# Optimization experiments

Hardware: AMD Instinct MI355X
Metric: run time of the kernel (lower is better)

## Reference

```python
import jax, jax.numpy as jnp
import numpy as np

BATCH, D_IN, D_OUT = 2048, 1024, 4096


def setup_inputs() -> dict:
    key = jax.random.key(0)
    kx, kw = jax.random.split(key)
    x = jax.random.normal(kx, (BATCH, D_IN), dtype=jnp.float32)
    W = jax.random.normal(kw, (D_IN, D_OUT), dtype=jnp.float32)  # nn.Parameter init: N(0,1)
    return {"x": x, "W": W}


def reference(x, W):
    # out[b,o] = -1/2 * sum_i (x[b,i] - W[i,o])^2
    # instead of materializing the [B, O, I] broadcast tensor.
    x_sq = jnp.sum(x * x, axis=1, keepdims=True)          # [B, 1]
    w_sq = jnp.sum(W * W, axis=0, keepdims=True)          # [1, O]
    xw = jnp.matmul(x, W)                                  # [B, O] GEMM
    return -0.5 * (x_sq - 2.0 * xw + w_sq)
```

## Files before the change

kernel.cpp:

```cpp
#include <hip/hip_runtime.h>
#include <stdint.h>

#define BATCH 2048
#define DIN   1024
#define DOUT  4096


__device__ __forceinline__ ushort f2bf(float f) {
    uint32_t u = __float_as_uint(f);
    u += 0x7fffu + ((u >> 16) & 1u);
    return (ushort)(u >> 16);
}

__device__ __forceinline__ void async_copy16(const void* gsrc, void* ldst) {
    __builtin_amdgcn_global_load_lds(
        reinterpret_cast<uint32_t __attribute__((address_space(1)))*>(
            reinterpret_cast<uintptr_t>(gsrc)),
        reinterpret_cast<uint32_t __attribute__((address_space(3)))*>(
            reinterpret_cast<uintptr_t>(ldst)),
        16, 0, 0);
}

typedef __bf16 bf16x8 __attribute__((ext_vector_type(8)));
typedef float  f32x4  __attribute__((ext_vector_type(4)));

__global__ __launch_bounds__(256) void prep_fused(const float* __restrict__ x,
                                                  const float* __restrict__ W,
                                                  ushort* __restrict__ xb,
                                                  float* __restrict__ xsq,
                                                  ushort* __restrict__ wbt,
                                                  float* __restrict__ wsqp) {
    __shared__ float tile[64][65];
    const int b = blockIdx.x;
    if (b < 256) {
        const int o0 = (b >> 2) * 64;
        const int jb = b & 3;
        const int tx = threadIdx.x & 63;
        const int ty = threadIdx.x >> 6;
        float ssq = 0.f;
        for (int sub = 0; sub < 4; ++sub) {
            const int i0 = jb * 256 + sub * 64;
            if (sub) __syncthreads();
            #pragma unroll
            for (int r = ty; r < 64; r += 4) {
                const float v = W[(size_t)(i0 + r) * DOUT + o0 + tx];
                tile[r][tx] = v;
                ssq += v * v;
            }
            __syncthreads();
            #pragma unroll
            for (int r = ty; r < 64; r += 4)
                wbt[(size_t)(o0 + r) * DIN + i0 + tx] = f2bf(tile[tx][r]);
        }
        __syncthreads();
        tile[ty][tx] = ssq;
        __syncthreads();
        if (ty == 0)
            wsqp[(size_t)jb * DOUT + o0 + tx] =
                tile[0][tx] + tile[1][tx] + tile[2][tx] + tile[3][tx];
    } else {
        const int blk  = b - 256;
        const int wv   = threadIdx.x >> 6;
        const int lane = threadIdx.x & 63;
        #pragma unroll
        for (int rr = 0; rr < 4; ++rr) {
            const int row = blk * 16 + wv * 4 + rr;
            const float4* src = (const float4*)(x + (size_t)row * DIN);
            ushort4* dst = (ushort4*)(xb + (size_t)row * DIN);
            float s = 0.f;
            #pragma unroll
            for (int c = 0; c < 4; ++c) {
                const float4 v = src[c * 64 + lane];
                ushort4 pk;
                pk.x = f2bf(v.x); pk.y = f2bf(v.y);
                pk.z = f2bf(v.z); pk.w = f2bf(v.w);
                dst[c * 64 + lane] = pk;
                s += v.x * v.x + v.y * v.y + v.z * v.z + v.w * v.w;
            }
            #pragma unroll
            for (int off = 32; off > 0; off >>= 1) s += __shfl_down(s, off);
            if (lane == 0) xsq[row] = s;
        }
    }
}

#define BM 128
#define BN 128
#define BK 64

__global__ __launch_bounds__(256, 2) void gemm_bt_epi(
    const ushort* __restrict__ A,
    const ushort* __restrict__ Bt,
    const float* __restrict__ xsq,
    const float* __restrict__ wsqp,
    float* __restrict__ out) {
    __shared__ __align__(16) ushort sA[BM * BK];
    __shared__ __align__(16) ushort sB[BN * BK];

    const int tid  = threadIdx.x;
    const int wv   = tid >> 6;
    const int lane = tid & 63;
    const int wr = wv >> 1, wc = wv & 1;

    const int bid  = blockIdx.x;
    const int xcd  = bid & 7;
    const int slot = bid >> 3;
    const int nb   = xcd * 4 + (slot & 3);
    const int mb   = slot >> 2;
    const int m0 = mb * BM;
    const int n0 = nb * BN;

    const int st_row = wv * 32 + (lane >> 3);
    const int st_c   = ((((lane & 7) - (lane >> 3)) & 7)) * 8;

    const ushort* agp = A  + (size_t)(m0 + st_row) * DIN + st_c;
    const ushort* bgp = Bt + (size_t)(n0 + st_row) * DIN + st_c;

    f32x4 acc[4][4] = {};

    const int a_row = wr * 64 + (lane & 15);
    const int b_row = wc * 64 + (lane & 15);
    int kpos[2];
    #pragma unroll
    for (int kk = 0; kk < 2; ++kk)
        kpos[kk] = ((((lane >> 4) + 4 * kk + (lane & 7)) & 7)) * 8;

    for (int kt = 0; kt < DIN; kt += BK) {
        __syncthreads();
        #pragma unroll
        for (int q = 0; q < 4; ++q)
            async_copy16(agp + (size_t)q * 8 * DIN + kt, &sA[wv * 2048 + q * 512]);
        #pragma unroll
        for (int q = 0; q < 4; ++q)
            async_copy16(bgp + (size_t)q * 8 * DIN + kt, &sB[wv * 2048 + q * 512]);
        __syncthreads();

        #pragma unroll
        for (int kk = 0; kk < 2; ++kk) {
            bf16x8 fa[4], fb[4];
            #pragma unroll
            for (int i = 0; i < 4; ++i)
                fa[i] = *(const bf16x8*)&sA[(a_row + i * 16) * BK + kpos[kk]];
            #pragma unroll
            for (int i = 0; i < 4; ++i)
                fb[i] = *(const bf16x8*)&sB[(b_row + i * 16) * BK + kpos[kk]];
            #pragma unroll
            for (int mi = 0; mi < 4; ++mi)
                #pragma unroll
                for (int ni = 0; ni < 4; ++ni)
                    acc[mi][ni] = __builtin_amdgcn_mfma_f32_16x16x32_bf16(
                        fa[mi], fb[ni], acc[mi][ni], 0, 0, 0);
        }
    }

    const int er = (lane >> 4) * 4;
    const int ec = lane & 15;
    float wh[4];
    #pragma unroll
    for (int ni = 0; ni < 4; ++ni) {
        const int col = n0 + wc * 64 + ni * 16 + ec;
        wh[ni] = 0.5f * (wsqp[col] + wsqp[DOUT + col] +
                         wsqp[2 * DOUT + col] + wsqp[3 * DOUT + col]);
    }
    #pragma unroll
    for (int mi = 0; mi < 4; ++mi) {
        const int row = m0 + wr * 64 + mi * 16 + er;
        #pragma unroll
        for (int r = 0; r < 4; ++r) {
            const float xh = 0.5f * xsq[row + r];
            #pragma unroll
            for (int ni = 0; ni < 4; ++ni) {
                const int col = n0 + wc * 64 + ni * 16 + ec;
                out[(size_t)(row + r) * DOUT + col] = acc[mi][ni][r] - xh - wh[ni];
            }
        }
    }
}


extern "C" void kernel_launch(void* const* d_in, const int* in_sizes, int n_in,
                              void* d_out, int out_size, void* d_ws, size_t ws_size,
                              hipStream_t stream) {
    const float* x = (const float*)d_in[0];
    const float* W = (const float*)d_in[1];
    float* out = (float*)d_out;

    char* ws = (char*)d_ws;
    ushort* xb   = (ushort*)ws;
    ushort* wbt  = (ushort*)(ws + (4u << 20));
    float*  xsq  = (float*)(ws + (12u << 20));
    float*  wsqp = (float*)(ws + (12u << 20) + (32u << 10));

    prep_fused<<<384, 256, 0, stream>>>(x, W, xb, xsq, wbt, wsqp);
    gemm_bt_epi<<<512, 256, 0, stream>>>(xb, wbt, xsq, wsqp, out);
}
```

Before: 113.9 us.

## Load B fragments directly from global into registers with double buffering

The B tile no longer goes through LDS. Each wave loads its B MFMA fragments straight from global memory into registers, double-buffered one K-step ahead, while only A still goes through LDS. This halves LDS use and traffic and overlaps the B loads with MFMA work. In exchange, B global reads are no longer shared between the two waves in a row pair, so global and L2 traffic for B doubles, the uncoalesced 16-byte row-strided loads may be inefficient, and register pressure rises against the 2-blocks-per-SM launch bound.

```diff
diff --git a/kernel.cpp b/kernel.cpp
--- a/kernel.cpp
+++ b/kernel.cpp
@@ -95,7 +95,6 @@
     const float* __restrict__ wsqp,
     float* __restrict__ out) {
     __shared__ __align__(16) ushort sA[BM * BK];
-    __shared__ __align__(16) ushort sB[BN * BK];
 
     const int tid  = threadIdx.x;
     const int wv   = tid >> 6;
@@ -112,44 +111,84 @@
 
     const int st_row = wv * 32 + (lane >> 3);
     const int st_c   = ((((lane & 7) - (lane >> 3)) & 7)) * 8;
-
-    const ushort* agp = A  + (size_t)(m0 + st_row) * DIN + st_c;
-    const ushort* bgp = Bt + (size_t)(n0 + st_row) * DIN + st_c;
+    const ushort* agp = A + (size_t)(m0 + st_row) * DIN + st_c;
+
+    const ushort* bq = Bt + (size_t)(n0 + wc * 64 + (lane & 15)) * DIN
+                          + ((lane >> 4) * 8);
 
     f32x4 acc[4][4] = {};
 
     const int a_row = wr * 64 + (lane & 15);
-    const int b_row = wc * 64 + (lane & 15);
     int kpos[2];
     #pragma unroll
     for (int kk = 0; kk < 2; ++kk)
         kpos[kk] = ((((lane >> 4) + 4 * kk + (lane & 7)) & 7)) * 8;
 
-    for (int kt = 0; kt < DIN; kt += BK) {
+    bf16x8 b0[2][4], b1[2][4];
+    #pragma unroll
+    for (int kk = 0; kk < 2; ++kk)
+        #pragma unroll
+        for (int ni = 0; ni < 4; ++ni)
+            b0[kk][ni] = *(const bf16x8*)(bq + (size_t)ni * 16 * DIN + kk * 32);
+
+    for (int kt = 0; kt < DIN; kt += 2 * BK) {
         __syncthreads();
         #pragma unroll
         for (int q = 0; q < 4; ++q)
             async_copy16(agp + (size_t)q * 8 * DIN + kt, &sA[wv * 2048 + q * 512]);
-        #pragma unroll
-        for (int q = 0; q < 4; ++q)
-            async_copy16(bgp + (size_t)q * 8 * DIN + kt, &sB[wv * 2048 + q * 512]);
-        __syncthreads();
-
+        __syncthreads();
+
+        {
+            const int ktn = kt + BK;
+            #pragma unroll
+            for (int kk = 0; kk < 2; ++kk)
+                #pragma unroll
+                for (int ni = 0; ni < 4; ++ni)
+                    b1[kk][ni] = *(const bf16x8*)(bq + (size_t)ni * 16 * DIN +
+                                                  ktn + kk * 32);
+        }
         #pragma unroll
         for (int kk = 0; kk < 2; ++kk) {
-            bf16x8 fa[4], fb[4];
+            bf16x8 fa[4];
             #pragma unroll
             for (int i = 0; i < 4; ++i)
                 fa[i] = *(const bf16x8*)&sA[(a_row + i * 16) * BK + kpos[kk]];
             #pragma unroll
+            for (int mi = 0; mi < 4; ++mi)
+                #pragma unroll
+                for (int ni = 0; ni < 4; ++ni)
+                    acc[mi][ni] = __builtin_amdgcn_mfma_f32_16x16x32_bf16(
+                        fa[mi], b0[kk][ni], acc[mi][ni], 0, 0, 0);
+        }
+
+        __syncthreads();
+        #pragma unroll
+        for (int q = 0; q < 4; ++q)
+            async_copy16(agp + (size_t)q * 8 * DIN + kt + BK,
+                         &sA[wv * 2048 + q * 512]);
+        __syncthreads();
+
+        {
+            const int ktn = (kt + 2 * BK < DIN) ? kt + 2 * BK : 0;
+            #pragma unroll
+            for (int kk = 0; kk < 2; ++kk)
+                #pragma unroll
+                for (int ni = 0; ni < 4; ++ni)
+                    b0[kk][ni] = *(const bf16x8*)(bq + (size_t)ni * 16 * DIN +
+                                                  ktn + kk * 32);
+        }
+        #pragma unroll
+        for (int kk = 0; kk < 2; ++kk) {
+            bf16x8 fa[4];
+            #pragma unroll
             for (int i = 0; i < 4; ++i)
-                fb[i] = *(const bf16x8*)&sB[(b_row + i * 16) * BK + kpos[kk]];
+                fa[i] = *(const bf16x8*)&sA[(a_row + i * 16) * BK + kpos[kk]];
             #pragma unroll
             for (int mi = 0; mi < 4; ++mi)
                 #pragma unroll
                 for (int ni = 0; ni < 4; ++ni)
                     acc[mi][ni] = __builtin_amdgcn_mfma_f32_16x16x32_bf16(
-                        fa[mi], fb[ni], acc[mi][ni], 0, 0, 0);
+                        fa[mi], b1[kk][ni], acc[mi][ni], 0, 0, 0);
         }
     }
 
```

Measured after the change: 132.4 us. +16.2%, slower.

## Double-buffer GEMM LDS tiles and vectorize transposed weight stores

Applied to the files above, without the earlier changes.

The GEMM main loop now uses two LDS buffers and issues the async global-to-LDS loads for the next K tile before computing on the current one, with one barrier per iteration. The goal is to hide global load latency behind MFMA work. LDS use doubles to 64KB per block, which may limit the two-blocks-per-CU occupancy. Separately, the weight transpose in the prep kernel writes packed 4-element bf16 vectors instead of scalar ushorts.

```diff
diff --git a/kernel.cpp b/kernel.cpp
--- a/kernel.cpp
+++ b/kernel.cpp
@@ -49,8 +49,16 @@
             }
             __syncthreads();
             #pragma unroll
-            for (int r = ty; r < 64; r += 4)
-                wbt[(size_t)(o0 + r) * DIN + i0 + tx] = f2bf(tile[tx][r]);
+            for (int p = 0; p < 4; ++p) {
+                const int o  = p * 16 + (threadIdx.x >> 4);
+                const int ch = threadIdx.x & 15;
+                ushort4 pk;
+                pk.x = f2bf(tile[ch * 4 + 0][o]);
+                pk.y = f2bf(tile[ch * 4 + 1][o]);
+                pk.z = f2bf(tile[ch * 4 + 2][o]);
+                pk.w = f2bf(tile[ch * 4 + 3][o]);
+                *(ushort4*)(wbt + (size_t)(o0 + o) * DIN + i0 + ch * 4) = pk;
+            }
         }
         __syncthreads();
         tile[ty][tx] = ssq;
@@ -94,8 +102,8 @@
     const float* __restrict__ xsq,
     const float* __restrict__ wsqp,
     float* __restrict__ out) {
-    __shared__ __align__(16) ushort sA[BM * BK];
-    __shared__ __align__(16) ushort sB[BN * BK];
+    __shared__ __align__(16) ushort sA[2 * BM * BK];
+    __shared__ __align__(16) ushort sB[2 * BN * BK];
 
     const int tid  = threadIdx.x;
     const int wv   = tid >> 6;
@@ -125,25 +133,40 @@
     for (int kk = 0; kk < 2; ++kk)
         kpos[kk] = ((((lane >> 4) + 4 * kk + (lane & 7)) & 7)) * 8;
 
+    #pragma unroll
+    for (int q = 0; q < 4; ++q)
+        async_copy16(agp + (size_t)q * 8 * DIN, &sA[wv * 2048 + q * 512]);
+    #pragma unroll
+    for (int q = 0; q < 4; ++q)
+        async_copy16(bgp + (size_t)q * 8 * DIN, &sB[wv * 2048 + q * 512]);
+    __syncthreads();
+
+    int cur = 0;
     for (int kt = 0; kt < DIN; kt += BK) {
-        __syncthreads();
-        #pragma unroll
-        for (int q = 0; q < 4; ++q)
-            async_copy16(agp + (size_t)q * 8 * DIN + kt, &sA[wv * 2048 + q * 512]);
-        #pragma unroll
-        for (int q = 0; q < 4; ++q)
-            async_copy16(bgp + (size_t)q * 8 * DIN + kt, &sB[wv * 2048 + q * 512]);
-        __syncthreads();
-
+        const int ktn = kt + BK;
+        if (ktn < DIN) {
+            const int nxt = (cur ^ 1) * 8192;
+            #pragma unroll
+            for (int q = 0; q < 4; ++q)
+                async_copy16(agp + (size_t)q * 8 * DIN + ktn,
+                             &sA[nxt + wv * 2048 + q * 512]);
+            #pragma unroll
+            for (int q = 0; q < 4; ++q)
+                async_copy16(bgp + (size_t)q * 8 * DIN + ktn,
+                             &sB[nxt + wv * 2048 + q * 512]);
+        }
+
+        const ushort* cA = &sA[cur * 8192];
+        const ushort* cB = &sB[cur * 8192];
         #pragma unroll
         for (int kk = 0; kk < 2; ++kk) {
             bf16x8 fa[4], fb[4];
             #pragma unroll
             for (int i = 0; i < 4; ++i)
-                fa[i] = *(const bf16x8*)&sA[(a_row + i * 16) * BK + kpos[kk]];
+                fa[i] = *(const bf16x8*)&cA[(a_row + i * 16) * BK + kpos[kk]];
             #pragma unroll
             for (int i = 0; i < 4; ++i)
-                fb[i] = *(const bf16x8*)&sB[(b_row + i * 16) * BK + kpos[kk]];
+                fb[i] = *(const bf16x8*)&cB[(b_row + i * 16) * BK + kpos[kk]];
             #pragma unroll
             for (int mi = 0; mi < 4; ++mi)
                 #pragma unroll
@@ -151,6 +174,9 @@
                     acc[mi][ni] = __builtin_amdgcn_mfma_f32_16x16x32_bf16(
                         fa[mi], fb[ni], acc[mi][ni], 0, 0, 0);
         }
+
+        __syncthreads();
+        cur ^= 1;
     }
 
     const int er = (lane >> 4) * 4;
```

New measurement: 112.0 us. Within noise of the previous version (-1.6%).
